# Kernel optimization log

Measured on AMD Instinct MI355X. Metric: run time of the kernel, lower is better.

## Reference

```python
import jax, jax.numpy as jnp
import numpy as np

BETA = 0.95
THRESH = 1.0
T = 25
MAXD = 11      # dilated_kernel_size: 250//25=10 -> bumped to odd 11
LP = 10        # left_pad = 250//25
B = 1024
SIGINIT = 5.0  # max_delay // 2, SIG is frozen at this value


@jax.custom_vjp
def atan_spike(u):
    # heaviside forward, atan surrogate gradient (snntorch surrogate.atan, alpha=2)
    return (u > 0).astype(u.dtype)

def _atan_fwd(u):
    return atan_spike(u), u

def _atan_bwd(u, g):
    return (g / (1.0 + (jnp.pi * u) ** 2),)

atan_spike.defvjp(_atan_fwd, _atan_bwd)


def dcls_kernel(W, P, SIG):
    # DCLS 'gauss': gaussian-interpolated dense kernel.
    # W: (O, I, kc), P/SIG: (1, O, I, kc) -> dense kernel (O, I, MAXD)
    idx = jnp.arange(MAXD, dtype=W.dtype)
    Pc = P[0] + MAXD // 2                      # center positions in dense kernel
    S = jnp.abs(SIG[0]) + 0.27                 # sigma floor (DCLS epsilon)
    X = jnp.exp(-0.5 * ((idx[:, None, None, None] - Pc) / S) ** 2)  # (K,O,I,kc)
    X = X / (X.sum(axis=0, keepdims=True) + 1e-7)
    return jnp.einsum('oic,joic->oij', W, X)


def dcls_conv(x, W, P, SIG, b):
    # x: (B, C_in, L) -> (B, C_out, L - MAXD + 1), VALID conv like padding=0
    k = dcls_kernel(W, P, SIG)
    y = jax.lax.conv_general_dilated(x, k, (1,), 'VALID',
                                     dimension_numbers=('NCH', 'OIH', 'NCH'))
    return y + b[None, :, None]


def batchnorm(x, gamma, beta, mean, var, eps=1e-5):
    # eval-mode BatchNorm1d over (B, C, L)
    inv = gamma / jnp.sqrt(var + eps)
    return (x - mean[None, :, None]) * inv[None, :, None] + beta[None, :, None]


def lif_scan(x):
    # snntorch Leaky, reset_mechanism='subtract'; x: (B, C, T) input currents
    xT = jnp.moveaxis(x, 2, 0)  # (T, B, C)

    def step(mem, xt):
        reset = jax.lax.stop_gradient(atan_spike(mem - THRESH))  # detached reset
        mem = BETA * mem + xt - reset * THRESH
        spk = atan_spike(mem - THRESH)
        return mem, (spk, mem)

    _, (spk, mem) = jax.lax.scan(step, jnp.zeros_like(xT[0]), xT)
    return spk, mem  # each (T, B, C)


def pad_left(x):
    return jnp.pad(x, ((0, 0), (0, 0), (LP, 0)))


def setup_inputs() -> dict:
    key = jax.random.key(0)
    ks = jax.random.split(key, 16)

    def w_init(k, o, i):
        return jax.random.normal(k, (o, i, 1), jnp.float32) / np.sqrt(i)

    inp = {
        'data': jax.random.normal(ks[0], (B, T, 140), jnp.float32),
        'W1': w_init(ks[1], 256, 140),
        'b1': jax.random.normal(ks[2], (256,), jnp.float32) * 0.01,
        'P1': jax.random.uniform(ks[3], (1, 256, 140, 1), jnp.float32, -SIGINIT, SIGINIT),
        'SIG1': jnp.full((1, 256, 140, 1), SIGINIT, jnp.float32),
        'bn1_gamma': jax.random.uniform(ks[4], (256,), jnp.float32, 0.5, 1.5),
        'bn1_beta': jax.random.normal(ks[5], (256,), jnp.float32) * 0.1,
        'bn1_mean': jax.random.normal(ks[6], (256,), jnp.float32) * 0.1,
        'bn1_var': jax.random.uniform(ks[7], (256,), jnp.float32, 0.5, 1.5),
        'W2': w_init(ks[8], 256, 256),
        'b2': jax.random.normal(ks[9], (256,), jnp.float32) * 0.01,
        'P2': jax.random.uniform(ks[10], (1, 256, 256, 1), jnp.float32, -SIGINIT, SIGINIT),
        'SIG2': jnp.full((1, 256, 256, 1), SIGINIT, jnp.float32),
        'bn2_gamma': jax.random.uniform(ks[11], (256,), jnp.float32, 0.5, 1.5),
        'bn2_beta': jax.random.normal(ks[12], (256,), jnp.float32) * 0.1,
        'bn2_mean': jax.random.normal(ks[13], (256,), jnp.float32) * 0.1,
        'bn2_var': jax.random.uniform(ks[14], (256,), jnp.float32, 0.5, 1.5),
        'W3': w_init(ks[15], 20, 256),
        'b3': jnp.zeros((20,), jnp.float32),
        'P3': jax.random.uniform(jax.random.fold_in(key, 99), (1, 20, 256, 1), jnp.float32, -SIGINIT, SIGINIT),
        'SIG3': jnp.full((1, 20, 256, 1), SIGINIT, jnp.float32),
    }
    return inp


def reference(data, W1, b1, P1, SIG1, bn1_gamma, bn1_beta, bn1_mean, bn1_var,
              W2, b2, P2, SIG2, bn2_gamma, bn2_beta, bn2_mean, bn2_var,
              W3, b3, P3, SIG3):
    # data: (B, T, 140); pad time dim on the left, then to (B, C, L)
    x = jnp.moveaxis(jnp.pad(data, ((0, 0), (LP, 0), (0, 0))), 1, 2)  # (B,140,T+LP)
    x = batchnorm(dcls_conv(x, W1, P1, SIG1, b1), bn1_gamma, bn1_beta, bn1_mean, bn1_var)
    spk1, _ = lif_scan(x)                  # (T, B, 256)
    in1 = jnp.moveaxis(spk1, 0, 2)         # (B, 256, T)  (dropout eval = identity)

    x = batchnorm(dcls_conv(pad_left(in1), W2, P2, SIG2, b2),
                  bn2_gamma, bn2_beta, bn2_mean, bn2_var)
    spk2, _ = lif_scan(x)
    in2 = jnp.moveaxis(spk2, 0, 2)         # (B, 256, T)

    x = dcls_conv(pad_left(in2), W3, P3, SIG3, b3)  # (B, 20, T)
    spk3, mem3 = lif_scan(x)               # (T, B, 20) each
    return spk3, mem3
```

## Files before the change

kernel.cpp:

```cpp
#include <hip/hip_runtime.h>
#include <math.h>

#define BB 1024
#define TT 25
#define LP 10
#define MAXD 11

#define XR2 26
#define XC 264
#define XSZ2 (XR2 * XC)

#define IC1 140
#define ICP1 160
#define XC1 168
#define XSZ1 (XR2 * XC1)
#define SS1 (2 * XSZ1)

typedef __bf16 bf16x8 __attribute__((ext_vector_type(8)));
typedef float  f32x4  __attribute__((ext_vector_type(4)));

#define MFMA16(A, B, C) __builtin_amdgcn_mfma_f32_16x16x32_bf16((A), (B), (C), 0, 0, 0)

__global__ void gen_trip(const float* __restrict__ W,
                         const float* __restrict__ P,
                         const float* __restrict__ SIG,
                         __bf16* __restrict__ Khi, __bf16* __restrict__ Kmid,
                         __bf16* __restrict__ Klo,
                         int O, int Opad, int I, int Ipad) {
    int idx = blockIdx.x * blockDim.x + threadIdx.x;
    if (idx >= Opad * Ipad) return;
    int i = idx % Ipad;
    int o = idx / Ipad;
    if (o >= O || i >= I) {
#pragma unroll
        for (int j = 0; j < MAXD; ++j) {
            size_t ofs = ((size_t)(j * Opad + o)) * Ipad + i;
            Khi[ofs] = (__bf16)0.0f;
            Kmid[ofs] = (__bf16)0.0f;
            Klo[ofs] = (__bf16)0.0f;
        }
        return;
    }
    int widx = o * I + i;
    float w  = W[widx];
    float pc = P[widx] + (float)(MAXD / 2);
    float s  = fabsf(SIG[widx]) + 0.27f;
    float x[MAXD];
    float sum = 0.f;
#pragma unroll
    for (int j = 0; j < MAXD; ++j) {
        float d = ((float)j - pc) / s;
        x[j] = expf(-0.5f * d * d);
        sum += x[j];
    }
    float denom = sum + 1e-7f;
#pragma unroll
    for (int j = 0; j < MAXD; ++j) {
        float kv = w * (x[j] / denom);
        __bf16 h = (__bf16)kv;
        float  r1 = kv - (float)h;
        __bf16 m = (__bf16)r1;
        float  r2 = r1 - (float)m;
        __bf16 l = (__bf16)r2;
        size_t ofs = ((size_t)(j * Opad + o)) * Ipad + i;
        Khi[ofs] = h;
        Kmid[ofs] = m;
        Klo[ofs] = l;
    }
}

__global__ __launch_bounds__(512, 2)
void conv1_mfma(const float* __restrict__ xin,
                const __bf16* __restrict__ Khi,
                const __bf16* __restrict__ Kmid,
                const __bf16* __restrict__ Klo,
                const float* __restrict__ bias,
                const float* __restrict__ gamma,
                const float* __restrict__ beta,
                const float* __restrict__ mean,
                const float* __restrict__ var,
                __bf16* __restrict__ spk1) {
    __shared__ __align__(16) char smem[3 * SS1 * 2];
    __bf16* xs = (__bf16*)smem;
    float*  ys = (float*)smem;

    const int b0   = blockIdx.x * 2;
    const int tid  = threadIdx.x;
    const int w    = tid >> 6;
    const int lane = tid & 63;
    const int lm   = lane & 15;
    const int quad = lane >> 4;

    {
        uint32_t* xz = (uint32_t*)smem;
        for (int k = tid; k < 3 * SS1 / 2; k += 512) xz[k] = 0u;
    }
    __syncthreads();
#pragma unroll
    for (int bl = 0; bl < 2; ++bl) {
        const float* src = xin + (size_t)(b0 + bl) * (TT * IC1);
        for (int k = tid; k < TT * IC1; k += 512) {
            int t = k / IC1;
            int i = k - t * IC1;
            float x  = src[k];
            __bf16 h = (__bf16)x;
            float r1 = x - (float)h;
            __bf16 m = (__bf16)r1;
            float r2 = r1 - (float)m;
            __bf16 l = (__bf16)r2;
            int ofs = bl * XSZ1 + t * XC1 + i;
            xs[0 * SS1 + ofs] = h;
            xs[1 * SS1 + ofs] = m;
            xs[2 * SS1 + ofs] = l;
        }
    }
    __syncthreads();

    f32x4 acc[2][4];
#pragma unroll
    for (int p = 0; p < 2; ++p)
#pragma unroll
        for (int nt = 0; nt < 4; ++nt) acc[p][nt] = (f32x4){0.f, 0.f, 0.f, 0.f};

    auto loadA = [&](int n, bf16x8* Ah, bf16x8* Am, bf16x8* Al) {
        n = (n > 54) ? 54 : n;
        const int j = n / 5;
        const int ic = n - 5 * j;
        const size_t base =
            (size_t)(j * 256 + w * 32 + lm) * ICP1 + ic * 32 + quad * 8;
#pragma unroll
        for (int p = 0; p < 2; ++p) {
            Ah[p] = *(const bf16x8*)(Khi  + base + p * 16 * ICP1);
            Am[p] = *(const bf16x8*)(Kmid + base + p * 16 * ICP1);
            Al[p] = *(const bf16x8*)(Klo  + base + p * 16 * ICP1);
        }
    };

    auto step = [&](int n, bf16x8* Ah, bf16x8* Am, bf16x8* Al) {
        const int j = n / 5;
        const int ic = n - 5 * j;
        int r0 = lm + j - 10;          r0 = ((unsigned)r0 < 25u) ? r0 : 25;
        int r1 = 16 + lm + j - 10;     r1 = ((unsigned)r1 < 25u) ? r1 : 25;
        const int col = ic * 32 + quad * 8;
#pragma unroll
        for (int bl = 0; bl < 2; ++bl) {
            bf16x8 Bh[2], Bm[2], Bl[2];
#pragma unroll
            for (int th = 0; th < 2; ++th) {
                const int row = th ? r1 : r0;
                const int ofs = bl * XSZ1 + row * XC1 + col;
                Bh[th] = *(const bf16x8*)&xs[0 * SS1 + ofs];
                Bm[th] = *(const bf16x8*)&xs[1 * SS1 + ofs];
                Bl[th] = *(const bf16x8*)&xs[2 * SS1 + ofs];
            }
#pragma unroll
            for (int p = 0; p < 2; ++p)
#pragma unroll
                for (int th = 0; th < 2; ++th)
                    acc[p][bl * 2 + th] = MFMA16(Ah[p], Bh[th], acc[p][bl * 2 + th]);
#pragma unroll
            for (int p = 0; p < 2; ++p)
#pragma unroll
                for (int th = 0; th < 2; ++th)
                    acc[p][bl * 2 + th] = MFMA16(Ah[p], Bm[th], acc[p][bl * 2 + th]);
#pragma unroll
            for (int p = 0; p < 2; ++p)
#pragma unroll
                for (int th = 0; th < 2; ++th)
                    acc[p][bl * 2 + th] = MFMA16(Am[p], Bh[th], acc[p][bl * 2 + th]);
#pragma unroll
            for (int p = 0; p < 2; ++p)
#pragma unroll
                for (int th = 0; th < 2; ++th)
                    acc[p][bl * 2 + th] = MFMA16(Ah[p], Bl[th], acc[p][bl * 2 + th]);
#pragma unroll
            for (int p = 0; p < 2; ++p)
#pragma unroll
                for (int th = 0; th < 2; ++th)
                    acc[p][bl * 2 + th] = MFMA16(Am[p], Bm[th], acc[p][bl * 2 + th]);
#pragma unroll
            for (int p = 0; p < 2; ++p)
#pragma unroll
                for (int th = 0; th < 2; ++th)
                    acc[p][bl * 2 + th] = MFMA16(Al[p], Bh[th], acc[p][bl * 2 + th]);
        }
    };

    bf16x8 A0h[2], A0m[2], A0l[2], A1h[2], A1m[2], A1l[2];
    loadA(0, A0h, A0m, A0l);
    for (int n = 0; n < 54; n += 2) {
        loadA(n + 1, A1h, A1m, A1l);
        step(n, A0h, A0m, A0l);
        loadA(n + 2, A0h, A0m, A0l);
        step(n + 1, A1h, A1m, A1l);
    }
    step(54, A0h, A0m, A0l);

#pragma unroll
    for (int bl = 0; bl < 2; ++bl) {
        __syncthreads();
#pragma unroll
        for (int p = 0; p < 2; ++p)
#pragma unroll
            for (int th = 0; th < 2; ++th) {
                int t = th * 16 + lm;
                if (t < TT) {
                    int ob = w * 32 + p * 16 + quad * 4;
#pragma unroll
                    for (int v = 0; v < 4; ++v)
                        ys[(ob + v) * 27 + t] = acc[p][bl * 2 + th][v];
                }
            }
        __syncthreads();
        if (tid < 256) {
            const int o = tid;
            float scale = gamma[o] / sqrtf(var[o] + 1e-5f);
            float ofs   = (bias[o] - mean[o]) * scale + beta[o];
            unsigned short* dst =
                (unsigned short*)spk1 + (size_t)(b0 + bl) * (TT * 256) + o;
            const float* yrow = &ys[o * 27];
            float memv = 0.f;
#pragma unroll
            for (int t = 0; t < TT; ++t) {
                float a     = yrow[t] * scale + ofs;
                float reset = (memv > 1.0f) ? 1.0f : 0.f;
                memv        = 0.95f * memv + a - reset;
                dst[t * 256] = (memv > 1.0f) ? 0x3F80 : 0;
            }
        }
    }
}

__global__ __launch_bounds__(512, 2)
void conv23_mfma(const __bf16* __restrict__ spk1,
                 const __bf16* __restrict__ Khi,
                 const __bf16* __restrict__ Kmid,
                 const __bf16* __restrict__ Klo,
                 const float* __restrict__ bias,
                 const float* __restrict__ gamma,
                 const float* __restrict__ beta,
                 const float* __restrict__ mean,
                 const float* __restrict__ var,
                 const __bf16* __restrict__ K3hi,
                 const __bf16* __restrict__ K3mid,
                 const __bf16* __restrict__ K3lo,
                 const float* __restrict__ b3,
                 float* __restrict__ out) {
    __shared__ __align__(16) char smem[61568];
    __bf16* xs  = (__bf16*)smem;
    float*  ysq = (float*)(smem + 54912);
    float*  ys3 = (float*)smem;

    const int b0   = blockIdx.x * 4;
    const int tid  = threadIdx.x;
    const int w    = tid >> 6;
    const int lane = tid & 63;
    const int lm   = lane & 15;
    const int quad = lane >> 4;

    for (int k = tid; k < 4 * (XC / 2); k += 512) {
        int bl = k / (XC / 2);
        int c  = k % (XC / 2);
        ((uint32_t*)xs)[(bl * XSZ2 + 25 * XC) / 2 + c] = 0u;
    }
    for (int k = tid; k < 4 * 800; k += 512) {
        int bl = k / 800;
        int v  = k % 800;
        int t  = v >> 5;
        int iv = v & 31;
        uint4 d = ((const uint4*)(spk1 + (size_t)(b0 + bl) * (TT * 256)))[v];
        *(uint4*)&xs[bl * XSZ2 + t * XC + iv * 8] = d;
    }
    __syncthreads();

    f32x4 acc[2][8];
#pragma unroll
    for (int pi = 0; pi < 2; ++pi)
#pragma unroll
        for (int nt = 0; nt < 8; ++nt) acc[pi][nt] = (f32x4){0.f, 0.f, 0.f, 0.f};

    {
        auto loadA = [&](int n, bf16x8* Ah, bf16x8* Am, bf16x8* Al) {
            n = (n > 87) ? 87 : n;
            const int j = n >> 3, ic = n & 7;
#pragma unroll
            for (int pi = 0; pi < 2; ++pi) {
                const size_t base =
                    (size_t)(j * 256 + w * 32 + pi * 16 + lm) * 256 + ic * 32 + quad * 8;
                Ah[pi] = *(const bf16x8*)(Khi  + base);
                Am[pi] = *(const bf16x8*)(Kmid + base);
                Al[pi] = *(const bf16x8*)(Klo  + base);
            }
        };
        auto loadB = [&](int n, bf16x8* Bf) {
            const int j = n >> 3, ic = n & 7;
            int r0 = lm + j - 10;          r0 = ((unsigned)r0 < 25u) ? r0 : 25;
            int r1 = 16 + lm + j - 10;     r1 = ((unsigned)r1 < 25u) ? r1 : 25;
            const int col = ic * 32 + quad * 8;
#pragma unroll
            for (int bl = 0; bl < 4; ++bl) {
                Bf[bl * 2 + 0] = *(const bf16x8*)&xs[bl * XSZ2 + r0 * XC + col];
                Bf[bl * 2 + 1] = *(const bf16x8*)&xs[bl * XSZ2 + r1 * XC + col];
            }
        };
        auto compute = [&](bf16x8* Ah, bf16x8* Am, bf16x8* Al, bf16x8* Bf) {
#pragma unroll
            for (int pi = 0; pi < 2; ++pi)
#pragma unroll
                for (int nt = 0; nt < 8; ++nt)
                    acc[pi][nt] = MFMA16(Ah[pi], Bf[nt], acc[pi][nt]);
#pragma unroll
            for (int pi = 0; pi < 2; ++pi)
#pragma unroll
                for (int nt = 0; nt < 8; ++nt)
                    acc[pi][nt] = MFMA16(Am[pi], Bf[nt], acc[pi][nt]);
#pragma unroll
            for (int pi = 0; pi < 2; ++pi)
#pragma unroll
                for (int nt = 0; nt < 8; ++nt)
                    acc[pi][nt] = MFMA16(Al[pi], Bf[nt], acc[pi][nt]);
        };

        bf16x8 A0h[2], A0m[2], A0l[2], A1h[2], A1m[2], A1l[2], B0[8], B1[8];
        loadA(0, A0h, A0m, A0l);
        loadB(0, B0);
        for (int n = 0; n < 86; n += 2) {
            loadA(n + 1, A1h, A1m, A1l);
            loadB(n + 1, B1);
            compute(A0h, A0m, A0l, B0);
            loadA(n + 2, A0h, A0m, A0l);
            loadB(n + 2, B0);
            compute(A1h, A1m, A1l, B1);
        }
        loadA(87, A1h, A1m, A1l);
        loadB(87, B1);
        compute(A0h, A0m, A0l, B0);
        compute(A1h, A1m, A1l, B1);
    }

#pragma unroll
    for (int bl = 0; bl < 4; ++bl) {
#pragma unroll
        for (int q = 0; q < 4; ++q) {
            __syncthreads();
            if ((w >> 1) == q) {
#pragma unroll
                for (int pi = 0; pi < 2; ++pi)
#pragma unroll
                    for (int th = 0; th < 2; ++th) {
                        int t = th * 16 + lm;
                        if (t < TT) {
                            int ol = (w & 1) * 32 + pi * 16 + quad * 4;
#pragma unroll
                            for (int v = 0; v < 4; ++v)
                                ysq[(ol + v) * 26 + t] = acc[pi][bl * 2 + th][v];
                        }
                    }
            }
            __syncthreads();
            if (tid < 64) {
                const int o = q * 64 + tid;
                float scale = gamma[o] / sqrtf(var[o] + 1e-5f);
                float ofs   = (bias[o] - mean[o]) * scale + beta[o];
                const float* yrow = &ysq[tid * 26];
                unsigned short* sx = (unsigned short*)xs;
                float memv = 0.f;
#pragma unroll
                for (int t = 0; t < TT; ++t) {
                    float a     = yrow[t] * scale + ofs;
                    float reset = (memv > 1.0f) ? 1.0f : 0.f;
                    memv        = 0.95f * memv + a - reset;
                    sx[bl * XSZ2 + t * XC + o] = (memv > 1.0f) ? 0x3F80 : 0;
                }
            }
        }
    }
    __syncthreads();

    {
        const int p3  = w >> 2;
        const int bl3 = w & 3;
        f32x4 accH[2], accM[2], accL[2];
#pragma unroll
        for (int th = 0; th < 2; ++th) {
            accH[th] = (f32x4){0.f, 0.f, 0.f, 0.f};
            accM[th] = (f32x4){0.f, 0.f, 0.f, 0.f};
            accL[th] = (f32x4){0.f, 0.f, 0.f, 0.f};
        }

        auto loadA3 = [&](int n, bf16x8* Ah, bf16x8* Am, bf16x8* Al) {
            n = (n > 87) ? 87 : n;
            const int j = n >> 3, ic = n & 7;
            const size_t kofs =
                ((size_t)(j * 32 + p3 * 16 + lm)) * 256 + ic * 32 + quad * 8;
            *Ah = *(const bf16x8*)(K3hi  + kofs);
            *Am = *(const bf16x8*)(K3mid + kofs);
            *Al = *(const bf16x8*)(K3lo  + kofs);
        };
        auto step3 = [&](int n, bf16x8 Ah, bf16x8 Am, bf16x8 Al) {
            const int j = n >> 3, ic = n & 7;
#pragma unroll
            for (int th = 0; th < 2; ++th) {
                int r = th * 16 + lm + j - 10;
                r = ((unsigned)r < 25u) ? r : 25;
                bf16x8 Bf =
                    *(const bf16x8*)&xs[bl3 * XSZ2 + r * XC + ic * 32 + quad * 8];
                accH[th] = MFMA16(Ah, Bf, accH[th]);
                accM[th] = MFMA16(Am, Bf, accM[th]);
                accL[th] = MFMA16(Al, Bf, accL[th]);
            }
        };

        bf16x8 A0h, A0m, A0l, A1h, A1m, A1l;
        loadA3(0, &A0h, &A0m, &A0l);
        for (int n = 0; n < 86; n += 2) {
            loadA3(n + 1, &A1h, &A1m, &A1l);
            step3(n, A0h, A0m, A0l);
            loadA3(n + 2, &A0h, &A0m, &A0l);
            step3(n + 1, A1h, A1m, A1l);
        }
        loadA3(87, &A1h, &A1m, &A1l);
        step3(86, A0h, A0m, A0l);
        step3(87, A1h, A1m, A1l);

        __syncthreads();
#pragma unroll
        for (int th = 0; th < 2; ++th) {
            int t = th * 16 + lm;
            if (t < TT) {
#pragma unroll
                for (int v = 0; v < 4; ++v)
                    ys3[(bl3 * 32 + p3 * 16 + quad * 4 + v) * 26 + t] =
                        accH[th][v] + accM[th][v] + accL[th][v];
            }
        }
        __syncthreads();

        if (tid < 80) {
            const int bl2 = tid / 20;
            const int o   = tid % 20;
            float memv = 0.f;
            float bo   = b3[o];
            const float* yrow = &ys3[(bl2 * 32 + o) * 26];
#pragma unroll
            for (int t = 0; t < TT; ++t) {
                float a     = yrow[t] + bo;
                float reset = (memv > 1.0f) ? 1.0f : 0.f;
                memv        = 0.95f * memv + a - reset;
                float spk   = (memv > 1.0f) ? 1.0f : 0.f;
                out[(t * BB + (b0 + bl2)) * 20 + o]               = spk;
                out[TT * BB * 20 + (t * BB + (b0 + bl2)) * 20 + o] = memv;
            }
        }
    }
}

extern "C" void kernel_launch(void* const* d_in, const int* in_sizes, int n_in,
                              void* d_out, int out_size, void* d_ws, size_t ws_size,
                              hipStream_t stream) {
    const float* data = (const float*)d_in[0];
    const float* W1   = (const float*)d_in[1];
    const float* b1   = (const float*)d_in[2];
    const float* P1   = (const float*)d_in[3];
    const float* SIG1 = (const float*)d_in[4];
    const float* g1   = (const float*)d_in[5];
    const float* be1  = (const float*)d_in[6];
    const float* m1   = (const float*)d_in[7];
    const float* v1   = (const float*)d_in[8];
    const float* W2   = (const float*)d_in[9];
    const float* b2   = (const float*)d_in[10];
    const float* P2   = (const float*)d_in[11];
    const float* SIG2 = (const float*)d_in[12];
    const float* g2   = (const float*)d_in[13];
    const float* be2  = (const float*)d_in[14];
    const float* m2   = (const float*)d_in[15];
    const float* v2   = (const float*)d_in[16];
    const float* W3   = (const float*)d_in[17];
    const float* b3   = (const float*)d_in[18];
    const float* P3   = (const float*)d_in[19];
    const float* SIG3 = (const float*)d_in[20];
    float* out = (float*)d_out;

    char* p = (char*)d_ws;
    __bf16* K1hi  = (__bf16*)p;  p += 901120;
    __bf16* K1mid = (__bf16*)p;  p += 901120;
    __bf16* K1lo  = (__bf16*)p;  p += 901120;
    __bf16* spk1  = (__bf16*)p;  p += 13107200;
    __bf16* K2hi  = (__bf16*)p;  p += 1441792;
    __bf16* K2mid = (__bf16*)p;  p += 1441792;
    __bf16* K2lo  = (__bf16*)p;  p += 1441792;
    __bf16* K3hi  = (__bf16*)p;  p += 180224;
    __bf16* K3mid = (__bf16*)p;  p += 180224;
    __bf16* K3lo  = (__bf16*)p;

    gen_trip<<<(256 * 160 + 255) / 256, 256, 0, stream>>>(
        W1, P1, SIG1, K1hi, K1mid, K1lo, 256, 256, 140, 160);
    gen_trip<<<(256 * 256 + 255) / 256, 256, 0, stream>>>(
        W2, P2, SIG2, K2hi, K2mid, K2lo, 256, 256, 256, 256);
    gen_trip<<<(32 * 256 + 255) / 256, 256, 0, stream>>>(
        W3, P3, SIG3, K3hi, K3mid, K3lo, 20, 32, 256, 256);

    conv1_mfma<<<BB / 2, 512, 0, stream>>>(data, K1hi, K1mid, K1lo,
                                           b1, g1, be1, m1, v1, spk1);
    conv23_mfma<<<BB / 4, 512, 0, stream>>>(spk1, K2hi, K2mid, K2lo,
                                            b2, g2, be2, m2, v2,
                                            K3hi, K3mid, K3lo, b3, out);
}
```

Baseline: 435.6 us.

## Split conv2/conv3 work across 16 waves per block instead of 8

Doubles the conv23 block size to 1024 threads, so each wave computes one 16-row output-channel tile instead of two in conv2. In conv3 each wave handles one time half instead of both. This halves per-wave accumulator and A-fragment registers and adds latency hiding within a block. In exchange, each wave's B fragments from shared memory are reused across only one A tile, which doubles LDS read traffic per MFMA. Launch bounds (1024,4) also constrain registers tightly, which could cause spills; only 256 blocks are launched.

```diff
diff --git a/kernel.cpp b/kernel.cpp
--- a/kernel.cpp
+++ b/kernel.cpp
@@ -231,7 +231,7 @@
     }
 }
 
-__global__ __launch_bounds__(512, 2)
+__global__ __launch_bounds__(1024, 4)
 void conv23_mfma(const __bf16* __restrict__ spk1,
                  const __bf16* __restrict__ Khi,
                  const __bf16* __restrict__ Kmid,
@@ -258,12 +258,12 @@
     const int lm   = lane & 15;
     const int quad = lane >> 4;
 
-    for (int k = tid; k < 4 * (XC / 2); k += 512) {
+    for (int k = tid; k < 4 * (XC / 2); k += 1024) {
         int bl = k / (XC / 2);
         int c  = k % (XC / 2);
         ((uint32_t*)xs)[(bl * XSZ2 + 25 * XC) / 2 + c] = 0u;
     }
-    for (int k = tid; k < 4 * 800; k += 512) {
+    for (int k = tid; k < 4 * 800; k += 1024) {
         int bl = k / 800;
         int v  = k % 800;
         int t  = v >> 5;
@@ -273,24 +273,19 @@
     }
     __syncthreads();
 
-    f32x4 acc[2][8];
-#pragma unroll
-    for (int pi = 0; pi < 2; ++pi)
-#pragma unroll
-        for (int nt = 0; nt < 8; ++nt) acc[pi][nt] = (f32x4){0.f, 0.f, 0.f, 0.f};
+    f32x4 acc[8];
+#pragma unroll
+    for (int nt = 0; nt < 8; ++nt) acc[nt] = (f32x4){0.f, 0.f, 0.f, 0.f};
 
     {
         auto loadA = [&](int n, bf16x8* Ah, bf16x8* Am, bf16x8* Al) {
             n = (n > 87) ? 87 : n;
             const int j = n >> 3, ic = n & 7;
-#pragma unroll
-            for (int pi = 0; pi < 2; ++pi) {
-                const size_t base =
-                    (size_t)(j * 256 + w * 32 + pi * 16 + lm) * 256 + ic * 32 + quad * 8;
-                Ah[pi] = *(const bf16x8*)(Khi  + base);
-                Am[pi] = *(const bf16x8*)(Kmid + base);
-                Al[pi] = *(const bf16x8*)(Klo  + base);
-            }
+            const size_t base =
+                (size_t)(j * 256 + w * 16 + lm) * 256 + ic * 32 + quad * 8;
+            *Ah = *(const bf16x8*)(Khi  + base);
+            *Am = *(const bf16x8*)(Kmid + base);
+            *Al = *(const bf16x8*)(Klo  + base);
         };
         auto loadB = [&](int n, bf16x8* Bf) {
             const int j = n >> 3, ic = n & 7;
@@ -303,36 +298,27 @@
                 Bf[bl * 2 + 1] = *(const bf16x8*)&xs[bl * XSZ2 + r1 * XC + col];
             }
         };
-        auto compute = [&](bf16x8* Ah, bf16x8* Am, bf16x8* Al, bf16x8* Bf) {
-#pragma unroll
-            for (int pi = 0; pi < 2; ++pi)
-#pragma unroll
-                for (int nt = 0; nt < 8; ++nt)
-                    acc[pi][nt] = MFMA16(Ah[pi], Bf[nt], acc[pi][nt]);
-#pragma unroll
-            for (int pi = 0; pi < 2; ++pi)
-#pragma unroll
-                for (int nt = 0; nt < 8; ++nt)
-                    acc[pi][nt] = MFMA16(Am[pi], Bf[nt], acc[pi][nt]);
-#pragma unroll
-            for (int pi = 0; pi < 2; ++pi)
-#pragma unroll
-                for (int nt = 0; nt < 8; ++nt)
-                    acc[pi][nt] = MFMA16(Al[pi], Bf[nt], acc[pi][nt]);
+        auto compute = [&](bf16x8 Ah, bf16x8 Am, bf16x8 Al, bf16x8* Bf) {
+#pragma unroll
+            for (int nt = 0; nt < 8; ++nt) acc[nt] = MFMA16(Ah, Bf[nt], acc[nt]);
+#pragma unroll
+            for (int nt = 0; nt < 8; ++nt) acc[nt] = MFMA16(Am, Bf[nt], acc[nt]);
+#pragma unroll
+            for (int nt = 0; nt < 8; ++nt) acc[nt] = MFMA16(Al, Bf[nt], acc[nt]);
         };
 
-        bf16x8 A0h[2], A0m[2], A0l[2], A1h[2], A1m[2], A1l[2], B0[8], B1[8];
-        loadA(0, A0h, A0m, A0l);
+        bf16x8 A0h, A0m, A0l, A1h, A1m, A1l, B0[8], B1[8];
+        loadA(0, &A0h, &A0m, &A0l);
         loadB(0, B0);
         for (int n = 0; n < 86; n += 2) {
-            loadA(n + 1, A1h, A1m, A1l);
+            loadA(n + 1, &A1h, &A1m, &A1l);
             loadB(n + 1, B1);
             compute(A0h, A0m, A0l, B0);
-            loadA(n + 2, A0h, A0m, A0l);
+            loadA(n + 2, &A0h, &A0m, &A0l);
             loadB(n + 2, B0);
             compute(A1h, A1m, A1l, B1);
         }
-        loadA(87, A1h, A1m, A1l);
+        loadA(87, &A1h, &A1m, &A1l);
         loadB(87, B1);
         compute(A0h, A0m, A0l, B0);
         compute(A1h, A1m, A1l, B1);
@@ -343,19 +329,17 @@
 #pragma unroll
         for (int q = 0; q < 4; ++q) {
             __syncthreads();
-            if ((w >> 1) == q) {
-#pragma unroll
-                for (int pi = 0; pi < 2; ++pi)
-#pragma unroll
-                    for (int th = 0; th < 2; ++th) {
-                        int t = th * 16 + lm;
-                        if (t < TT) {
-                            int ol = (w & 1) * 32 + pi * 16 + quad * 4;
-#pragma unroll
-                            for (int v = 0; v < 4; ++v)
-                                ysq[(ol + v) * 26 + t] = acc[pi][bl * 2 + th][v];
-                        }
+            if ((w >> 2) == q) {
+#pragma unroll
+                for (int th = 0; th < 2; ++th) {
+                    int t = th * 16 + lm;
+                    if (t < TT) {
+                        int ol = (w & 3) * 16 + quad * 4;
+#pragma unroll
+                        for (int v = 0; v < 4; ++v)
+                            ysq[(ol + v) * 26 + t] = acc[bl * 2 + th][v];
                     }
+                }
             }
             __syncthreads();
             if (tid < 64) {
@@ -378,15 +362,12 @@
     __syncthreads();
 
     {
-        const int p3  = w >> 2;
-        const int bl3 = w & 3;
-        f32x4 accH[2], accM[2], accL[2];
-#pragma unroll
-        for (int th = 0; th < 2; ++th) {
-            accH[th] = (f32x4){0.f, 0.f, 0.f, 0.f};
-            accM[th] = (f32x4){0.f, 0.f, 0.f, 0.f};
-            accL[th] = (f32x4){0.f, 0.f, 0.f, 0.f};
-        }
+        const int p3  = w >> 3;
+        const int bl3 = (w >> 1) & 3;
+        const int th3 = w & 1;
+        f32x4 accH = (f32x4){0.f, 0.f, 0.f, 0.f};
+        f32x4 accM = (f32x4){0.f, 0.f, 0.f, 0.f};
+        f32x4 accL = (f32x4){0.f, 0.f, 0.f, 0.f};
 
         auto loadA3 = [&](int n, bf16x8* Ah, bf16x8* Am, bf16x8* Al) {
             n = (n > 87) ? 87 : n;
@@ -399,16 +380,13 @@
         };
         auto step3 = [&](int n, bf16x8 Ah, bf16x8 Am, bf16x8 Al) {
             const int j = n >> 3, ic = n & 7;
-#pragma unroll
-            for (int th = 0; th < 2; ++th) {
-                int r = th * 16 + lm + j - 10;
-                r = ((unsigned)r < 25u) ? r : 25;
-                bf16x8 Bf =
-                    *(const bf16x8*)&xs[bl3 * XSZ2 + r * XC + ic * 32 + quad * 8];
-                accH[th] = MFMA16(Ah, Bf, accH[th]);
-                accM[th] = MFMA16(Am, Bf, accM[th]);
-                accL[th] = MFMA16(Al, Bf, accL[th]);
-            }
+            int r = th3 * 16 + lm + j - 10;
+            r = ((unsigned)r < 25u) ? r : 25;
+            bf16x8 Bf =
+                *(const bf16x8*)&xs[bl3 * XSZ2 + r * XC + ic * 32 + quad * 8];
+            accH = MFMA16(Ah, Bf, accH);
+            accM = MFMA16(Am, Bf, accM);
+            accL = MFMA16(Al, Bf, accL);
         };
 
         bf16x8 A0h, A0m, A0l, A1h, A1m, A1l;
@@ -424,14 +402,13 @@
         step3(87, A1h, A1m, A1l);
 
         __syncthreads();
-#pragma unroll
-        for (int th = 0; th < 2; ++th) {
-            int t = th * 16 + lm;
+        {
+            int t = th3 * 16 + lm;
             if (t < TT) {
 #pragma unroll
                 for (int v = 0; v < 4; ++v)
                     ys3[(bl3 * 32 + p3 * 16 + quad * 4 + v) * 26 + t] =
-                        accH[th][v] + accM[th][v] + accL[th][v];
+                        accH[v] + accM[v] + accL[v];
             }
         }
         __syncthreads();
@@ -502,7 +479,7 @@
 
     conv1_mfma<<<BB / 2, 512, 0, stream>>>(data, K1hi, K1mid, K1lo,
                                            b1, g1, be1, m1, v1, spk1);
-    conv23_mfma<<<BB / 4, 512, 0, stream>>>(spk1, K2hi, K2mid, K2lo,
-                                            b2, g2, be2, m2, v2,
-                                            K3hi, K3mid, K3lo, b3, out);
+    conv23_mfma<<<BB / 4, 1024, 0, stream>>>(spk1, K2hi, K2mid, K2lo,
+                                             b2, g2, be2, m2, v2,
+                                             K3hi, K3mid, K3lo, b3, out);
 }
```

New measurement: 476.3 us. 9.3% more time.

## Process four batches per conv1 block and split fp32 inputs into bf16 on the fly

Applied to the files above, without the earlier changes.

conv1 now handles four batch elements per block instead of two, so each loaded bf16 triple-split weight fragment feeds twice as many MFMAs. The input tile is kept in LDS as fp32 rather than three pre-split bf16 planes, and the hi/mid/lo split is recomputed in registers at every B-operand load. This cuts global weight traffic and LDS footprint per batch. In exchange it adds per-step ALU work, doubles the accumulator registers (spill risk under the 512x2 launch bound), and halves the grid to 256 blocks, which lowers occupancy.

```diff
diff --git a/kernel.cpp b/kernel.cpp
--- a/kernel.cpp
+++ b/kernel.cpp
@@ -12,9 +12,9 @@
 
 #define IC1 140
 #define ICP1 160
-#define XC1 168
-#define XSZ1 (XR2 * XC1)
-#define SS1 (2 * XSZ1)
+#define XF_ROW 144
+#define XF_BATCH (XR2 * XF_ROW)
+#define XF_TOT (4 * XF_BATCH + 16)
 
 typedef __bf16 bf16x8 __attribute__((ext_vector_type(8)));
 typedef float  f32x4  __attribute__((ext_vector_type(4)));
@@ -80,47 +80,35 @@
                 const float* __restrict__ mean,
                 const float* __restrict__ var,
                 __bf16* __restrict__ spk1) {
-    __shared__ __align__(16) char smem[3 * SS1 * 2];
-    __bf16* xs = (__bf16*)smem;
-    float*  ys = (float*)smem;
-
-    const int b0   = blockIdx.x * 2;
+    __shared__ __align__(16) char smem[XF_TOT * 4];
+    float* xsf = (float*)smem;
+    float* ys  = (float*)smem;
+
+    const int b0   = blockIdx.x * 4;
     const int tid  = threadIdx.x;
     const int w    = tid >> 6;
     const int lane = tid & 63;
     const int lm   = lane & 15;
     const int quad = lane >> 4;
 
-    {
-        uint32_t* xz = (uint32_t*)smem;
-        for (int k = tid; k < 3 * SS1 / 2; k += 512) xz[k] = 0u;
-    }
+    for (int k = tid; k < XF_TOT; k += 512) xsf[k] = 0.f;
     __syncthreads();
 #pragma unroll
-    for (int bl = 0; bl < 2; ++bl) {
+    for (int bl = 0; bl < 4; ++bl) {
         const float* src = xin + (size_t)(b0 + bl) * (TT * IC1);
         for (int k = tid; k < TT * IC1; k += 512) {
             int t = k / IC1;
             int i = k - t * IC1;
-            float x  = src[k];
-            __bf16 h = (__bf16)x;
-            float r1 = x - (float)h;
-            __bf16 m = (__bf16)r1;
-            float r2 = r1 - (float)m;
-            __bf16 l = (__bf16)r2;
-            int ofs = bl * XSZ1 + t * XC1 + i;
-            xs[0 * SS1 + ofs] = h;
-            xs[1 * SS1 + ofs] = m;
-            xs[2 * SS1 + ofs] = l;
+            xsf[bl * XF_BATCH + t * XF_ROW + i] = src[k];
         }
     }
     __syncthreads();
 
-    f32x4 acc[2][4];
+    f32x4 acc[2][8];
 #pragma unroll
     for (int p = 0; p < 2; ++p)
 #pragma unroll
-        for (int nt = 0; nt < 4; ++nt) acc[p][nt] = (f32x4){0.f, 0.f, 0.f, 0.f};
+        for (int nt = 0; nt < 8; ++nt) acc[p][nt] = (f32x4){0.f, 0.f, 0.f, 0.f};
 
     auto loadA = [&](int n, bf16x8* Ah, bf16x8* Am, bf16x8* Al) {
         n = (n > 54) ? 54 : n;
@@ -143,15 +131,25 @@
         int r1 = 16 + lm + j - 10;     r1 = ((unsigned)r1 < 25u) ? r1 : 25;
         const int col = ic * 32 + quad * 8;
 #pragma unroll
-        for (int bl = 0; bl < 2; ++bl) {
+        for (int bl = 0; bl < 4; ++bl) {
             bf16x8 Bh[2], Bm[2], Bl[2];
 #pragma unroll
             for (int th = 0; th < 2; ++th) {
                 const int row = th ? r1 : r0;
-                const int ofs = bl * XSZ1 + row * XC1 + col;
-                Bh[th] = *(const bf16x8*)&xs[0 * SS1 + ofs];
-                Bm[th] = *(const bf16x8*)&xs[1 * SS1 + ofs];
-                Bl[th] = *(const bf16x8*)&xs[2 * SS1 + ofs];
+                const float* bp = &xsf[bl * XF_BATCH + row * XF_ROW + col];
+                float xv[8];
+                *(float4*)&xv[0] = *(const float4*)bp;
+                *(float4*)&xv[4] = *(const float4*)(bp + 4);
+#pragma unroll
+                for (int e = 0; e < 8; ++e) {
+                    __bf16 h = (__bf16)xv[e];
+                    float  q1 = xv[e] - (float)h;
+                    __bf16 m = (__bf16)q1;
+                    float  q2 = q1 - (float)m;
+                    Bh[th][e] = h;
+                    Bm[th][e] = m;
+                    Bl[th][e] = (__bf16)q2;
+                }
             }
 #pragma unroll
             for (int p = 0; p < 2; ++p)
@@ -197,7 +195,7 @@
     step(54, A0h, A0m, A0l);
 
 #pragma unroll
-    for (int bl = 0; bl < 2; ++bl) {
+    for (int bl = 0; bl < 4; ++bl) {
         __syncthreads();
 #pragma unroll
         for (int p = 0; p < 2; ++p)
@@ -500,7 +498,7 @@
     gen_trip<<<(32 * 256 + 255) / 256, 256, 0, stream>>>(
         W3, P3, SIG3, K3hi, K3mid, K3lo, 20, 32, 256, 256);
 
-    conv1_mfma<<<BB / 2, 512, 0, stream>>>(data, K1hi, K1mid, K1lo,
+    conv1_mfma<<<BB / 4, 512, 0, stream>>>(data, K1hi, K1mid, K1lo,
                                            b1, g1, be1, m1, v1, spk1);
     conv23_mfma<<<BB / 4, 512, 0, stream>>>(spk1, K2hi, K2mid, K2lo,
                                             b2, g2, be2, m2, v2,
```

Result: slower. 466.3 us (+7.1%).
